# Kernel tuning notes

Measured on AMD Instinct MI355X. Metric: run time of the kernel, lower is better.

The kernel has to match this reference:

```python
import jax, jax.numpy as jnp
import numpy as np

D = 1280      # emb_dim
H = 4         # n_heads
DH = D // H
FF = 256      # dim_feedforward / hidden_dim
NL = 2        # n_layers
B = 64        # number of graphs
N = 32768     # total tokens
L = 640       # max padded length (>= max graph size w.h.p.)
EPS = 1e-5


def setup_inputs() -> dict:
    key = jax.random.key(0)
    ks = jax.random.split(key, 24)
    s = 0.02
    x = jax.random.normal(ks[0], (N, D), jnp.float32)
    batch = jnp.sort(jax.random.randint(ks[1], (N,), 0, B))
    p = {
        "x": x, "batch": batch,
        # stacked per-layer transformer params (torch Linear convention: y = x @ W.T + b)
        "Wqkv": jax.random.normal(ks[2], (NL, 3 * D, D), jnp.float32) * s,
        "bqkv": jnp.zeros((NL, 3 * D), jnp.float32),
        "Wo":   jax.random.normal(ks[3], (NL, D, D), jnp.float32) * s,
        "bo":   jnp.zeros((NL, D), jnp.float32),
        "ln1w": jnp.ones((NL, D), jnp.float32),
        "ln1b": jnp.zeros((NL, D), jnp.float32),
        "W1":   jax.random.normal(ks[4], (NL, FF, D), jnp.float32) * s,
        "b1":   jnp.zeros((NL, FF), jnp.float32),
        "W2":   jax.random.normal(ks[5], (NL, D, FF), jnp.float32) * s,
        "b2":   jnp.zeros((NL, D), jnp.float32),
        "ln2w": jnp.ones((NL, D), jnp.float32),
        "ln2b": jnp.zeros((NL, D), jnp.float32),
        # final MLP: Linear(D,FF) -> ReLU -> Linear(FF,D)
        "Wm1": jax.random.normal(ks[6], (FF, D), jnp.float32) * s,
        "bm1": jnp.zeros((FF,), jnp.float32),
        "Wm2": jax.random.normal(ks[7], (D, FF), jnp.float32) * s,
        "bm2": jnp.zeros((D,), jnp.float32),
    }
    return p


def _ln(x, w, b):
    mu = jnp.mean(x, axis=-1, keepdims=True)
    var = jnp.var(x, axis=-1, keepdims=True)
    return (x - mu) * jax.lax.rsqrt(var + EPS) * w + b


def reference(x, batch, Wqkv, bqkv, Wo, bo, ln1w, ln1b, W1, b1, W2, b2,
              ln2w, ln2b, Wm1, bm1, Wm2, bm2):
    # --- graph_to_transformer_input: scatter ragged tokens into [B, L, D] ---
    counts = jax.ops.segment_sum(jnp.ones_like(batch), batch, num_segments=B)
    offsets = jnp.concatenate([jnp.zeros((1,), counts.dtype), jnp.cumsum(counts)[:-1]])
    pos = jnp.arange(N) - offsets[batch]                 # position within each graph
    padded = jnp.zeros((B, L, D), x.dtype).at[batch, pos].set(x)
    pad_mask = jnp.arange(L)[None, :] >= counts[:, None]  # True = padding key

    h = padded
    scale = 1.0 / np.sqrt(DH)
    for l in range(NL):  # post-norm TransformerEncoderLayer, relu, dropout=eval
        qkv = h @ Wqkv[l].T + bqkv[l]
        q, k, v = jnp.split(qkv, 3, axis=-1)
        sh = lambda t: t.reshape(B, L, H, DH).transpose(0, 2, 1, 3)  # [B,H,L,DH]
        q, k, v = sh(q), sh(k), sh(v)
        scores = jnp.einsum('bhqd,bhkd->bhqk', q, k) * scale
        scores = jnp.where(pad_mask[:, None, None, :], -1e9, scores)
        attn = jax.nn.softmax(scores, axis=-1)
        o = jnp.einsum('bhqk,bhkd->bhqd', attn, v).transpose(0, 2, 1, 3).reshape(B, L, D)
        o = o @ Wo[l].T + bo[l]
        h = _ln(h + o, ln1w[l], ln1b[l])
        ff = jax.nn.relu(h @ W1[l].T + b1[l]) @ W2[l].T + b2[l]
        h = _ln(h + ff, ln2w[l], ln2b[l])

    forces = jax.nn.relu(h @ Wm1.T + bm1) @ Wm2.T + bm2   # [B, L, D]
    return forces[batch, pos]                              # gather valid tokens -> [N, D]
```

## Files before the change

kernel.cpp:

```cpp
#include <hip/hip_runtime.h>

typedef unsigned short u16;
typedef __attribute__((ext_vector_type(8))) short bf16x8;
typedef __attribute__((ext_vector_type(4))) float f32x4;

#define N_TOK 32768
#define DIM   1280
#define NH    4
#define DH    320
#define FFD   256
#define NLAYER 2
#define NB    64
#define TD    3840
#define KVD   2560

#define GLD16(gp, lp) __builtin_amdgcn_global_load_lds( \
    (const __attribute__((address_space(1))) unsigned int*)(const void*)(gp), \
    (__attribute__((address_space(3))) unsigned int*)(void*)(lp), 16, 0, 0)

__device__ __forceinline__ float b2f(u16 v) {
    union { unsigned u; float f; } c; c.u = ((unsigned)v) << 16; return c.f;
}
__device__ __forceinline__ u16 f2b(float f) {
    union { float f; unsigned u; } c; c.f = f;
    unsigned r = c.u + 0x7fffu + ((c.u >> 16) & 1u);
    return (u16)(r >> 16);
}

__global__ __launch_bounds__(256) void k_f32_to_bf16(
    const float* __restrict__ in, u16* __restrict__ out, long n)
{
    long i = ((long)blockIdx.x * 256 + threadIdx.x) * 4;
    if (i >= n) return;
    float4 v = *(const float4*)&in[i];
    ushort4 o; o.x = f2b(v.x); o.y = f2b(v.y); o.z = f2b(v.z); o.w = f2b(v.w);
    *(ushort4*)&out[i] = o;
}

#define E0 9830400L
#define E1 13107200L
#define E2 13762560L
#define E3 14417920L
#define E4 14745600L
#define E5 15073280L
__global__ __launch_bounds__(256) void k_conv_weights(
    const float* __restrict__ Wqkv, const float* __restrict__ Wo,
    const float* __restrict__ W1,   const float* __restrict__ W2,
    const float* __restrict__ Wm1,  const float* __restrict__ Wm2,
    u16* __restrict__ d0, u16* __restrict__ d1, u16* __restrict__ d2,
    u16* __restrict__ d3, u16* __restrict__ d4, u16* __restrict__ d5)
{
    long i = ((long)blockIdx.x * 256 + threadIdx.x) * 4;
    if (i >= E5) return;
    const float* src; u16* dst; long off;
    if      (i < E0) { src = Wqkv; dst = d0; off = i; }
    else if (i < E1) { src = Wo;   dst = d1; off = i - E0; }
    else if (i < E2) { src = W1;   dst = d2; off = i - E1; }
    else if (i < E3) { src = W2;   dst = d3; off = i - E2; }
    else if (i < E4) { src = Wm1;  dst = d4; off = i - E3; }
    else             { src = Wm2;  dst = d5; off = i - E4; }
    float4 v = *(const float4*)&src[off];
    ushort4 o; o.x = f2b(v.x); o.y = f2b(v.y); o.z = f2b(v.z); o.w = f2b(v.w);
    *(ushort4*)&dst[off] = o;
}

__global__ void k_offsets(const int* __restrict__ batch, int* __restrict__ offs) {
    int b = threadIdx.x;
    if (b > NB) return;
    int lo = 0, hi = N_TOK;
    while (lo < hi) {
        int mid = (lo + hi) >> 1;
        if (batch[mid] < b) lo = mid + 1; else hi = mid;
    }
    offs[b] = lo;
}

__global__ __launch_bounds__(256) void k_gemm_mfma(
    const u16* __restrict__ A, int lda,
    const u16* __restrict__ W,
    const float* __restrict__ bias,
    void* __restrict__ Cv, int ldc,
    int K, int relu, int store_f32)
{
    __shared__ u16 Asm[128 * 64];
    __shared__ u16 Bsm[128 * 64];
    const int t    = threadIdx.x;
    const int lane = t & 63;
    const int w    = t >> 6;
    const int wr   = w >> 1, wc = w & 1;
    const long mBase = (long)blockIdx.y * 128;
    const long nBase = (long)blockIdx.x * 128;
    const int srow = lane >> 3;
    const int scol = (lane & 7) * 8;

    f32x4 acc[4][4];
    #pragma unroll
    for (int m = 0; m < 4; ++m)
        #pragma unroll
        for (int n = 0; n < 4; ++n) acc[m][n] = (f32x4){0.f, 0.f, 0.f, 0.f};

    for (int k0 = 0; k0 < K; k0 += 64) {
        __syncthreads();
        #pragma unroll
        for (int i = 0; i < 4; ++i) {
            const int c = w * 4 + i;
            const u16* ga = &A[(mBase + c * 8 + srow) * (long)lda + k0 + scol];
            const u16* gb = &W[(nBase + c * 8 + srow) * (long)K   + k0 + scol];
            GLD16(ga, &Asm[c * 512]);
            GLD16(gb, &Bsm[c * 512]);
        }
        __syncthreads();
        #pragma unroll
        for (int kk = 0; kk < 2; ++kk) {
            const int kc = kk * 32 + (lane >> 4) * 8;
            bf16x8 af[4], bfr[4];
            #pragma unroll
            for (int m = 0; m < 4; ++m)
                af[m] = *(const bf16x8*)&Asm[(wr * 64 + m * 16 + (lane & 15)) * 64 + kc];
            #pragma unroll
            for (int n = 0; n < 4; ++n)
                bfr[n] = *(const bf16x8*)&Bsm[(wc * 64 + n * 16 + (lane & 15)) * 64 + kc];
            #pragma unroll
            for (int m = 0; m < 4; ++m)
                #pragma unroll
                for (int n = 0; n < 4; ++n)
                    acc[m][n] = __builtin_amdgcn_mfma_f32_16x16x32_bf16(
                        af[m], bfr[n], acc[m][n], 0, 0, 0);
        }
    }

    const int ccol  = lane & 15;
    const int crow0 = (lane >> 4) * 4;
    #pragma unroll
    for (int m = 0; m < 4; ++m) {
        #pragma unroll
        for (int n = 0; n < 4; ++n) {
            const long col = nBase + wc * 64 + n * 16 + ccol;
            const float bv = bias[col];
            #pragma unroll
            for (int r = 0; r < 4; ++r) {
                const long row = mBase + wr * 64 + m * 16 + crow0 + r;
                float v = acc[m][n][r] + bv;
                if (relu) v = fmaxf(v, 0.f);
                if (store_f32) ((float*)Cv)[row * (long)ldc + col] = v;
                else           ((u16*)Cv)[row * (long)ldc + col] = f2b(v);
            }
        }
    }
}

__global__ __launch_bounds__(256) void k_gemm_qkv(
    const u16* __restrict__ A,
    const u16* __restrict__ W,
    const float* __restrict__ bias,
    u16* __restrict__ qd, u16* __restrict__ kvd)
{
    __shared__ u16 Asm[128 * 64];
    __shared__ u16 Bsm[128 * 64];
    const int t    = threadIdx.x;
    const int lane = t & 63;
    const int w    = t >> 6;
    const int wr   = w >> 1, wc = w & 1;
    const long mBase = (long)blockIdx.y * 128;
    const long nBase = (long)blockIdx.x * 128;
    const int srow = lane >> 3;
    const int scol = (lane & 7) * 8;

    f32x4 acc[4][4];
    #pragma unroll
    for (int m = 0; m < 4; ++m)
        #pragma unroll
        for (int n = 0; n < 4; ++n) acc[m][n] = (f32x4){0.f, 0.f, 0.f, 0.f};

    for (int k0 = 0; k0 < DIM; k0 += 64) {
        __syncthreads();
        #pragma unroll
        for (int i = 0; i < 4; ++i) {
            const int c = w * 4 + i;
            const u16* ga = &A[(mBase + c * 8 + srow) * (long)DIM + k0 + scol];
            const u16* gb = &W[(nBase + c * 8 + srow) * (long)DIM + k0 + scol];
            GLD16(ga, &Asm[c * 512]);
            GLD16(gb, &Bsm[c * 512]);
        }
        __syncthreads();
        #pragma unroll
        for (int kk = 0; kk < 2; ++kk) {
            const int kc = kk * 32 + (lane >> 4) * 8;
            bf16x8 af[4], bfr[4];
            #pragma unroll
            for (int m = 0; m < 4; ++m)
                af[m] = *(const bf16x8*)&Asm[(wr * 64 + m * 16 + (lane & 15)) * 64 + kc];
            #pragma unroll
            for (int n = 0; n < 4; ++n)
                bfr[n] = *(const bf16x8*)&Bsm[(wc * 64 + n * 16 + (lane & 15)) * 64 + kc];
            #pragma unroll
            for (int m = 0; m < 4; ++m)
                #pragma unroll
                for (int n = 0; n < 4; ++n)
                    acc[m][n] = __builtin_amdgcn_mfma_f32_16x16x32_bf16(
                        af[m], bfr[n], acc[m][n], 0, 0, 0);
        }
    }

    const int ccol  = lane & 15;
    const int crow0 = (lane >> 4) * 4;
    const bool isQ = (nBase < DIM);
    #pragma unroll
    for (int m = 0; m < 4; ++m) {
        #pragma unroll
        for (int n = 0; n < 4; ++n) {
            const long col = nBase + wc * 64 + n * 16 + ccol;
            const float bv = bias[col];
            #pragma unroll
            for (int r = 0; r < 4; ++r) {
                const long row = mBase + wr * 64 + m * 16 + crow0 + r;
                float v = acc[m][n][r] + bv;
                if (isQ) qd[row * (long)DIM + col]          = f2b(v);
                else     kvd[row * (long)KVD + (col - DIM)] = f2b(v);
            }
        }
    }
}

__global__ __launch_bounds__(256) void k_ln_residual(
    const u16* __restrict__ a, const u16* __restrict__ delta,
    const float* __restrict__ w, const float* __restrict__ bb,
    u16* __restrict__ out)
{
    const int lane = threadIdx.x & 63;
    const long row = (long)blockIdx.x * 4 + (threadIdx.x >> 6);
    const long base = row * DIM + lane * 20;
    float v[20];
    float s = 0.f, s2 = 0.f;
    #pragma unroll
    for (int k = 0; k < 5; ++k) {
        uint2 ua = *(const uint2*)&a[base + k * 4];
        uint2 ud = *(const uint2*)&delta[base + k * 4];
        u16 ah[4], dh[4];
        *(uint2*)ah = ua; *(uint2*)dh = ud;
        #pragma unroll
        for (int e = 0; e < 4; ++e) {
            float xv = b2f(ah[e]) + b2f(dh[e]);
            v[k * 4 + e] = xv; s += xv; s2 += xv * xv;
        }
    }
    #pragma unroll
    for (int off = 32; off > 0; off >>= 1) {
        s  += __shfl_xor(s, off);
        s2 += __shfl_xor(s2, off);
    }
    const float mu  = s * (1.f / DIM);
    const float var = s2 * (1.f / DIM) - mu * mu;
    const float inv = rsqrtf(fmaxf(var, 0.f) + 1e-5f);
    const int cb = lane * 20;
    #pragma unroll
    for (int k = 0; k < 5; ++k) {
        float4 wv = *(const float4*)&w[cb + k * 4];
        float4 bv = *(const float4*)&bb[cb + k * 4];
        u16 oh[4];
        oh[0] = f2b((v[k * 4 + 0] - mu) * inv * wv.x + bv.x);
        oh[1] = f2b((v[k * 4 + 1] - mu) * inv * wv.y + bv.y);
        oh[2] = f2b((v[k * 4 + 2] - mu) * inv * wv.z + bv.z);
        oh[3] = f2b((v[k * 4 + 3] - mu) * inv * wv.w + bv.w);
        *(uint2*)&out[base + k * 4] = *(uint2*)oh;
    }
}

__global__ __launch_bounds__(256) void k_attn_mfma(
    u16* __restrict__ q, const u16* __restrict__ kv, const int* __restrict__ offs)
{
    __shared__ u16 KV[21760];
    __shared__ float Ssm[32 * 65];
    __shared__ u16 Plds[32 * 72];
    __shared__ float mL[32], lL[32], aL[32];

    const int lin = blockIdx.x;
    const int gLo = lin & 7;
    const int j   = lin >> 3;
    const int g   = (j / 80) * 8 + gLo;
    const int rem = j % 80;
    const int hh  = rem / 20;
    const int qt  = rem % 20;

    const int gstart = offs[g];
    const int n = offs[g + 1] - gstart;
    if (qt * 32 >= n) return;
    const int nq = min(32, n - qt * 32);
    const int t    = threadIdx.x;
    const int lane = t & 63;
    const int w    = t >> 6;
    const int qr   = w >> 1, kr = w & 1;
    const int l15  = lane & 15;
    const int l4   = lane >> 4;
    const float scale = 0.05590169943749474f;

    if (t < 32) { mL[t] = -1e30f; lL[t] = 0.f; }

    bf16x8 qf[10];
    {
        int qrl = qt * 32 + qr * 16 + l15;
        if (qrl >= n) qrl = n - 1;
        const u16* gq = &q[(long)(gstart + qrl) * DIM + hh * DH + l4 * 8];
        #pragma unroll
        for (int c = 0; c < 10; ++c)
            qf[c] = *(const bf16x8*)&gq[c * 32];
    }

    f32x4 oacc[2][5];
    #pragma unroll
    for (int a = 0; a < 2; ++a)
        #pragma unroll
        for (int f = 0; f < 5; ++f) oacc[a][f] = (f32x4){0.f, 0.f, 0.f, 0.f};

    const int spos = t >> 3;
    const int sfb  = (t & 7) * 40;
    const int vpp  = t & 15;
    const int vfb  = (t >> 4) * 20;

    for (int kb = 0; kb < n; kb += 64) {
        const int nk = min(64, n - kb);
        __syncthreads();

        #pragma unroll
        for (int pass = 0; pass < 2; ++pass) {
            const int pos = spos + pass * 32;
            int gp = kb + pos; if (gp >= n) gp = n - 1;
            const u16* gk = &kv[(long)(gstart + gp) * KVD + hh * DH + sfb];
            uint4 c0 = *(const uint4*)(gk + 0);
            uint4 c1 = *(const uint4*)(gk + 8);
            uint4 c2 = *(const uint4*)(gk + 16);
            uint4 c3 = *(const uint4*)(gk + 24);
            uint4 c4 = *(const uint4*)(gk + 32);
            u16* dst = &KV[pos * 328 + sfb];
            *(uint4*)(dst + 0)  = c0;
            *(uint4*)(dst + 8)  = c1;
            *(uint4*)(dst + 16) = c2;
            *(uint4*)(dst + 24) = c3;
            *(uint4*)(dst + 32) = c4;
        }
        __syncthreads();

        #pragma unroll
        for (int kk = 0; kk < 2; ++kk) {
            const int colb = kr * 32 + kk * 16;
            f32x4 sacc = (f32x4){0.f, 0.f, 0.f, 0.f};
            #pragma unroll
            for (int c = 0; c < 10; ++c) {
                bf16x8 kf = *(const bf16x8*)&KV[(colb + l15) * 328 + c * 32 + l4 * 8];
                sacc = __builtin_amdgcn_mfma_f32_16x16x32_bf16(qf[c], kf, sacc, 0, 0, 0);
            }
            const int col = colb + l15;
            const int srow0 = qr * 16 + l4 * 4;
            const bool masked = (col >= nk);
            #pragma unroll
            for (int r = 0; r < 4; ++r)
                Ssm[(srow0 + r) * 65 + col] = masked ? -1e30f : sacc[r] * scale;
        }
        __syncthreads();

        {
            uint2 va4[2][5], vb4[2][5];
            #pragma unroll
            for (int pass = 0; pass < 2; ++pass) {
                int pr = vpp + pass * 16;
                int p0 = kb + 2 * pr, p1 = p0 + 1;
                if (p0 >= n) p0 = n - 1;
                if (p1 >= n) p1 = n - 1;
                const u16* g0 = &kv[(long)(gstart + p0) * KVD + DIM + hh * DH + vfb];
                const u16* g1 = &kv[(long)(gstart + p1) * KVD + DIM + hh * DH + vfb];
                #pragma unroll
                for (int i = 0; i < 5; ++i) {
                    va4[pass][i] = *(const uint2*)(g0 + i * 4);
                    vb4[pass][i] = *(const uint2*)(g1 + i * 4);
                }
            }

            const int r  = t >> 3;
            const int cg = (t & 7) * 8;
            float4 sa = *(const float4*)&Ssm[r * 65 + cg];
            float4 sb = *(const float4*)&Ssm[r * 65 + cg + 4];
            float mx = fmaxf(fmaxf(fmaxf(sa.x, sa.y), fmaxf(sa.z, sa.w)),
                             fmaxf(fmaxf(sb.x, sb.y), fmaxf(sb.z, sb.w)));
            mx = fmaxf(mx, __shfl_xor(mx, 1));
            mx = fmaxf(mx, __shfl_xor(mx, 2));
            mx = fmaxf(mx, __shfl_xor(mx, 4));
            const float mo = mL[r];
            const float mn = fmaxf(mo, mx);
            float p0f = __expf(sa.x - mn), p1f = __expf(sa.y - mn);
            float p2f = __expf(sa.z - mn), p3f = __expf(sa.w - mn);
            float p4f = __expf(sb.x - mn), p5f = __expf(sb.y - mn);
            float p6f = __expf(sb.z - mn), p7f = __expf(sb.w - mn);
            union { u16 h[8]; uint4 u; } pw;
            pw.h[0] = f2b(p0f); pw.h[1] = f2b(p1f); pw.h[2] = f2b(p2f); pw.h[3] = f2b(p3f);
            pw.h[4] = f2b(p4f); pw.h[5] = f2b(p5f); pw.h[6] = f2b(p6f); pw.h[7] = f2b(p7f);
            *(uint4*)&Plds[r * 72 + cg] = pw.u;
            float rs = ((p0f + p1f) + (p2f + p3f)) + ((p4f + p5f) + (p6f + p7f));
            rs += __shfl_xor(rs, 1);
            rs += __shfl_xor(rs, 2);
            rs += __shfl_xor(rs, 4);
            if ((t & 7) == 0) {
                const float al = __expf(mo - mn);
                aL[r] = al;
                lL[r] = lL[r] * al + rs;
                mL[r] = mn;
            }
            #pragma unroll
            for (int pass = 0; pass < 2; ++pass) {
                const int colp = 2 * (vpp + pass * 16);
                #pragma unroll
                for (int i = 0; i < 5; ++i) {
                    const unsigned a0 = va4[pass][i].x, a1 = va4[pass][i].y;
                    const unsigned b0 = vb4[pass][i].x, b1 = vb4[pass][i].y;
                    const int fb = vfb + i * 4;
                    *(unsigned*)&KV[(fb + 0) * 68 + colp] = (a0 & 0xffffu) | (b0 << 16);
                    *(unsigned*)&KV[(fb + 1) * 68 + colp] = (a0 >> 16) | (b0 & 0xffff0000u);
                    *(unsigned*)&KV[(fb + 2) * 68 + colp] = (a1 & 0xffffu) | (b1 << 16);
                    *(unsigned*)&KV[(fb + 3) * 68 + colp] = (a1 >> 16) | (b1 & 0xffff0000u);
                }
            }
        }
        __syncthreads();

        {
            float al[2][4];
            #pragma unroll
            for (int a = 0; a < 2; ++a)
                #pragma unroll
                for (int r = 0; r < 4; ++r)
                    al[a][r] = aL[a * 16 + l4 * 4 + r];
            #pragma unroll
            for (int a = 0; a < 2; ++a)
                #pragma unroll
                for (int f = 0; f < 5; ++f)
                    #pragma unroll
                    for (int r = 0; r < 4; ++r)
                        oacc[a][f][r] *= al[a][r];
            #pragma unroll
            for (int ks = 0; ks < 2; ++ks) {
                #pragma unroll
                for (int a = 0; a < 2; ++a) {
                    bf16x8 pf = *(const bf16x8*)&Plds[(a * 16 + l15) * 72 + ks * 32 + l4 * 8];
                    #pragma unroll
                    for (int f = 0; f < 5; ++f) {
                        const int fe = w * 80 + f * 16 + l15;
                        union { bf16x8 v; uint2 u[2]; } uv;
                        uv.u[0] = *(const uint2*)&KV[fe * 68 + ks * 32 + l4 * 8];
                        uv.u[1] = *(const uint2*)&KV[fe * 68 + ks * 32 + l4 * 8 + 4];
                        oacc[a][f] = __builtin_amdgcn_mfma_f32_16x16x32_bf16(
                            pf, uv.v, oacc[a][f], 0, 0, 0);
                    }
                }
            }
        }
    }

    float invl[2][4];
    #pragma unroll
    for (int a = 0; a < 2; ++a)
        #pragma unroll
        for (int r = 0; r < 4; ++r)
            invl[a][r] = 1.f / lL[a * 16 + l4 * 4 + r];
    #pragma unroll
    for (int a = 0; a < 2; ++a) {
        #pragma unroll
        for (int f = 0; f < 5; ++f) {
            #pragma unroll
            for (int r = 0; r < 4; ++r) {
                const int lrow = a * 16 + l4 * 4 + r;
                if (lrow < nq) {
                    const long grow = (long)(gstart + qt * 32 + lrow);
                    q[grow * DIM + hh * DH + w * 80 + f * 16 + l15] =
                        f2b(oacc[a][f][r] * invl[a][r]);
                }
            }
        }
    }
}

extern "C" void kernel_launch(void* const* d_in, const int* in_sizes, int n_in,
                              void* d_out, int out_size, void* d_ws, size_t ws_size,
                              hipStream_t stream) {
    const float* x     = (const float*)d_in[0];
    const int*   batch = (const int*)d_in[1];
    const float* Wqkv  = (const float*)d_in[2];
    const float* bqkv  = (const float*)d_in[3];
    const float* Wo    = (const float*)d_in[4];
    const float* bo    = (const float*)d_in[5];
    const float* ln1w  = (const float*)d_in[6];
    const float* ln1b  = (const float*)d_in[7];
    const float* W1    = (const float*)d_in[8];
    const float* b1    = (const float*)d_in[9];
    const float* W2    = (const float*)d_in[10];
    const float* b2    = (const float*)d_in[11];
    const float* ln2w  = (const float*)d_in[12];
    const float* ln2b  = (const float*)d_in[13];
    const float* Wm1   = (const float*)d_in[14];
    const float* bm1   = (const float*)d_in[15];
    const float* Wm2   = (const float*)d_in[16];
    const float* bm2   = (const float*)d_in[17];

    float* outF = (float*)d_out;
    u16*   qbuf = (u16*)d_out;

    char* ws   = (char*)d_ws;
    int*  offs = (int*)ws;
    u16*  h    = (u16*)(ws + 1024);
    u16*  kvb  = h + (size_t)N_TOK * DIM;
    u16*  tmp  = kvb;
    u16*  ff   = kvb + (size_t)N_TOK * DIM;
    u16*  wqkv_bf = kvb + (size_t)N_TOK * KVD;
    u16*  wo_bf   = wqkv_bf + (size_t)NLAYER * TD * DIM;
    u16*  w1_bf   = wo_bf   + (size_t)NLAYER * DIM * DIM;
    u16*  w2_bf   = w1_bf   + (size_t)NLAYER * FFD * DIM;
    u16*  wm1_bf  = w2_bf   + (size_t)NLAYER * DIM * FFD;
    u16*  wm2_bf  = wm1_bf  + (size_t)FFD * DIM;

    k_offsets<<<1, 128, 0, stream>>>(batch, offs);
    {
        long n = (long)N_TOK * DIM;
        k_f32_to_bf16<<<(int)(n / 1024), 256, 0, stream>>>(x, h, n);
        k_conv_weights<<<(int)(E5 / 1024), 256, 0, stream>>>(
            Wqkv, Wo, W1, W2, Wm1, Wm2,
            wqkv_bf, wo_bf, w1_bf, w2_bf, wm1_bf, wm2_bf);
    }

    dim3 blk(256);
    for (int l = 0; l < NLAYER; ++l) {
        const u16*   Wl = wqkv_bf + (size_t)l * TD * DIM;
        const float* bl = bqkv + (size_t)l * TD;
        k_gemm_qkv<<<dim3(TD / 128, N_TOK / 128), blk, 0, stream>>>(
            h, Wl, bl, qbuf, kvb);
        k_attn_mfma<<<dim3(20 * NH * NB), blk, 0, stream>>>(qbuf, kvb, offs);
        k_gemm_mfma<<<dim3(DIM / 128, N_TOK / 128), blk, 0, stream>>>(
            qbuf, DIM, wo_bf + (size_t)l * DIM * DIM, bo + (size_t)l * DIM,
            tmp, DIM, DIM, 0, 0);
        k_ln_residual<<<N_TOK / 4, blk, 0, stream>>>(
            h, tmp, ln1w + (size_t)l * DIM, ln1b + (size_t)l * DIM, h);
        k_gemm_mfma<<<dim3(FFD / 128, N_TOK / 128), blk, 0, stream>>>(
            h, DIM, w1_bf + (size_t)l * FFD * DIM, b1 + (size_t)l * FFD,
            ff, FFD, DIM, 1, 0);
        k_gemm_mfma<<<dim3(DIM / 128, N_TOK / 128), blk, 0, stream>>>(
            ff, FFD, w2_bf + (size_t)l * DIM * FFD, b2 + (size_t)l * DIM,
            tmp, DIM, FFD, 0, 0);
        k_ln_residual<<<N_TOK / 4, blk, 0, stream>>>(
            h, tmp, ln2w + (size_t)l * DIM, ln2b + (size_t)l * DIM, h);
    }
    k_gemm_mfma<<<dim3(FFD / 128, N_TOK / 128), blk, 0, stream>>>(
        h, DIM, wm1_bf, bm1, ff, FFD, DIM, 1, 0);
    k_gemm_mfma<<<dim3(DIM / 128, N_TOK / 128), blk, 0, stream>>>(
        ff, FFD, wm2_bf, bm2, outF, DIM, FFD, 0, 1);
}
```

Before: 2.643 ms.

## Double attention query tile to 64 rows with 512-thread blocks

The attention kernel now processes 64 query rows per block with 8 waves instead of 32 rows with 4 waves. Each wave pair handles a 16-row score slice, and the PV stage splits the waves into row halves and feature quarters. Each staged K/V tile is therefore reused across twice as many queries, which halves global K/V traffic and staging work per query. In exchange it needs more shared memory per block, which may lower occupancy, and ragged graph tails waste more work.

```diff
diff --git a/kernel.cpp b/kernel.cpp
--- a/kernel.cpp
+++ b/kernel.cpp
@@ -266,39 +266,40 @@
     }
 }
 
-__global__ __launch_bounds__(256) void k_attn_mfma(
+__global__ __launch_bounds__(512) void k_attn_mfma(
     u16* __restrict__ q, const u16* __restrict__ kv, const int* __restrict__ offs)
 {
     __shared__ u16 KV[21760];
-    __shared__ float Ssm[32 * 65];
-    __shared__ u16 Plds[32 * 72];
-    __shared__ float mL[32], lL[32], aL[32];
+    __shared__ float Ssm[64 * 65];
+    __shared__ u16 Plds[64 * 72];
+    __shared__ float mL[64], lL[64], aL[64];
 
     const int lin = blockIdx.x;
     const int gLo = lin & 7;
     const int j   = lin >> 3;
-    const int g   = (j / 80) * 8 + gLo;
-    const int rem = j % 80;
-    const int hh  = rem / 20;
-    const int qt  = rem % 20;
+    const int g   = (j / 40) * 8 + gLo;
+    const int rem = j % 40;
+    const int hh  = rem / 10;
+    const int qt  = rem % 10;
 
     const int gstart = offs[g];
     const int n = offs[g + 1] - gstart;
-    if (qt * 32 >= n) return;
-    const int nq = min(32, n - qt * 32);
+    if (qt * 64 >= n) return;
+    const int nq = min(64, n - qt * 64);
     const int t    = threadIdx.x;
     const int lane = t & 63;
     const int w    = t >> 6;
     const int qr   = w >> 1, kr = w & 1;
+    const int rh   = w >> 2, fs = w & 3;
     const int l15  = lane & 15;
     const int l4   = lane >> 4;
     const float scale = 0.05590169943749474f;
 
-    if (t < 32) { mL[t] = -1e30f; lL[t] = 0.f; }
+    if (t < 64) { mL[t] = -1e30f; lL[t] = 0.f; }
 
     bf16x8 qf[10];
     {
-        int qrl = qt * 32 + qr * 16 + l15;
+        int qrl = qt * 64 + qr * 16 + l15;
         if (qrl >= n) qrl = n - 1;
         const u16* gq = &q[(long)(gstart + qrl) * DIM + hh * DH + l4 * 8];
         #pragma unroll
@@ -314,24 +315,22 @@
 
     const int spos = t >> 3;
     const int sfb  = (t & 7) * 40;
-    const int vpp  = t & 15;
-    const int vfb  = (t >> 4) * 20;
+    const int vpp  = t & 31;
+    const int vfb  = (t >> 5) * 20;
 
     for (int kb = 0; kb < n; kb += 64) {
         const int nk = min(64, n - kb);
         __syncthreads();
 
-        #pragma unroll
-        for (int pass = 0; pass < 2; ++pass) {
-            const int pos = spos + pass * 32;
-            int gp = kb + pos; if (gp >= n) gp = n - 1;
+        {
+            int gp = kb + spos; if (gp >= n) gp = n - 1;
             const u16* gk = &kv[(long)(gstart + gp) * KVD + hh * DH + sfb];
             uint4 c0 = *(const uint4*)(gk + 0);
             uint4 c1 = *(const uint4*)(gk + 8);
             uint4 c2 = *(const uint4*)(gk + 16);
             uint4 c3 = *(const uint4*)(gk + 24);
             uint4 c4 = *(const uint4*)(gk + 32);
-            u16* dst = &KV[pos * 328 + sfb];
+            u16* dst = &KV[spos * 328 + sfb];
             *(uint4*)(dst + 0)  = c0;
             *(uint4*)(dst + 8)  = c1;
             *(uint4*)(dst + 16) = c2;
@@ -359,19 +358,17 @@
         __syncthreads();
 
         {
-            uint2 va4[2][5], vb4[2][5];
-            #pragma unroll
-            for (int pass = 0; pass < 2; ++pass) {
-                int pr = vpp + pass * 16;
-                int p0 = kb + 2 * pr, p1 = p0 + 1;
+            uint2 va4[5], vb4[5];
+            {
+                int p0 = kb + 2 * vpp, p1 = p0 + 1;
                 if (p0 >= n) p0 = n - 1;
                 if (p1 >= n) p1 = n - 1;
                 const u16* g0 = &kv[(long)(gstart + p0) * KVD + DIM + hh * DH + vfb];
                 const u16* g1 = &kv[(long)(gstart + p1) * KVD + DIM + hh * DH + vfb];
                 #pragma unroll
                 for (int i = 0; i < 5; ++i) {
-                    va4[pass][i] = *(const uint2*)(g0 + i * 4);
-                    vb4[pass][i] = *(const uint2*)(g1 + i * 4);
+                    va4[i] = *(const uint2*)(g0 + i * 4);
+                    vb4[i] = *(const uint2*)(g1 + i * 4);
                 }
             }
 
@@ -404,13 +401,12 @@
                 lL[r] = lL[r] * al + rs;
                 mL[r] = mn;
             }
-            #pragma unroll
-            for (int pass = 0; pass < 2; ++pass) {
-                const int colp = 2 * (vpp + pass * 16);
+            {
+                const int colp = 2 * vpp;
                 #pragma unroll
                 for (int i = 0; i < 5; ++i) {
-                    const unsigned a0 = va4[pass][i].x, a1 = va4[pass][i].y;
-                    const unsigned b0 = vb4[pass][i].x, b1 = vb4[pass][i].y;
+                    const unsigned a0 = va4[i].x, a1 = va4[i].y;
+                    const unsigned b0 = vb4[i].x, b1 = vb4[i].y;
                     const int fb = vfb + i * 4;
                     *(unsigned*)&KV[(fb + 0) * 68 + colp] = (a0 & 0xffffu) | (b0 << 16);
                     *(unsigned*)&KV[(fb + 1) * 68 + colp] = (a0 >> 16) | (b0 & 0xffff0000u);
@@ -427,7 +423,7 @@
             for (int a = 0; a < 2; ++a)
                 #pragma unroll
                 for (int r = 0; r < 4; ++r)
-                    al[a][r] = aL[a * 16 + l4 * 4 + r];
+                    al[a][r] = aL[rh * 32 + a * 16 + l4 * 4 + r];
             #pragma unroll
             for (int a = 0; a < 2; ++a)
                 #pragma unroll
@@ -439,10 +435,10 @@
             for (int ks = 0; ks < 2; ++ks) {
                 #pragma unroll
                 for (int a = 0; a < 2; ++a) {
-                    bf16x8 pf = *(const bf16x8*)&Plds[(a * 16 + l15) * 72 + ks * 32 + l4 * 8];
+                    bf16x8 pf = *(const bf16x8*)&Plds[(rh * 32 + a * 16 + l15) * 72 + ks * 32 + l4 * 8];
                     #pragma unroll
                     for (int f = 0; f < 5; ++f) {
-                        const int fe = w * 80 + f * 16 + l15;
+                        const int fe = fs * 80 + f * 16 + l15;
                         union { bf16x8 v; uint2 u[2]; } uv;
                         uv.u[0] = *(const uint2*)&KV[fe * 68 + ks * 32 + l4 * 8];
                         uv.u[1] = *(const uint2*)&KV[fe * 68 + ks * 32 + l4 * 8 + 4];
@@ -459,17 +455,17 @@
     for (int a = 0; a < 2; ++a)
         #pragma unroll
         for (int r = 0; r < 4; ++r)
-            invl[a][r] = 1.f / lL[a * 16 + l4 * 4 + r];
+            invl[a][r] = 1.f / lL[rh * 32 + a * 16 + l4 * 4 + r];
     #pragma unroll
     for (int a = 0; a < 2; ++a) {
         #pragma unroll
         for (int f = 0; f < 5; ++f) {
             #pragma unroll
             for (int r = 0; r < 4; ++r) {
-                const int lrow = a * 16 + l4 * 4 + r;
+                const int lrow = rh * 32 + a * 16 + l4 * 4 + r;
                 if (lrow < nq) {
-                    const long grow = (long)(gstart + qt * 32 + lrow);
-                    q[grow * DIM + hh * DH + w * 80 + f * 16 + l15] =
+                    const long grow = (long)(gstart + qt * 64 + lrow);
+                    q[grow * DIM + hh * DH + fs * 80 + f * 16 + l15] =
                         f2b(oacc[a][f][r] * invl[a][r]);
                 }
             }
@@ -530,7 +526,7 @@
         const float* bl = bqkv + (size_t)l * TD;
         k_gemm_qkv<<<dim3(TD / 128, N_TOK / 128), blk, 0, stream>>>(
             h, Wl, bl, qbuf, kvb);
-        k_attn_mfma<<<dim3(20 * NH * NB), blk, 0, stream>>>(qbuf, kvb, offs);
+        k_attn_mfma<<<dim3(10 * NH * NB), dim3(512), 0, stream>>>(qbuf, kvb, offs);
         k_gemm_mfma<<<dim3(DIM / 128, N_TOK / 128), blk, 0, stream>>>(
             qbuf, DIM, wo_bf + (size_t)l * DIM * DIM, bo + (size_t)l * DIM,
             tmp, DIM, DIM, 0, 0);
```

Result: faster. 2.574 ms, median of 3 (-2.6%).
